# Kernel tuning notes

Measured on AMD Instinct MI355X. Metric: run time of the kernel, lower is better.

Reference implementation:

```python
import jax, jax.numpy as jnp
import numpy as np

REG_MAX = 16
NC = 80
TOPK = 10
ALPHA = 1.0
BETA = 6.0
BOX_W, CLS_W, DFL_W = 7.5, 0.5, 1.5
IMG = 1280.0


def _ciou(b1, b2, eps=1e-7):
    # b1, b2: [..., 4] xyxy, broadcastable
    b1x1, b1y1, b1x2, b1y2 = b1[..., 0], b1[..., 1], b1[..., 2], b1[..., 3]
    b2x1, b2y1, b2x2, b2y2 = b2[..., 0], b2[..., 1], b2[..., 2], b2[..., 3]
    w1, h1 = b1x2 - b1x1, b1y2 - b1y1
    w2, h2 = b2x2 - b2x1, b2y2 - b2y1
    inter = (jnp.maximum(jnp.minimum(b1x2, b2x2) - jnp.maximum(b1x1, b2x1), 0.0) *
             jnp.maximum(jnp.minimum(b1y2, b2y2) - jnp.maximum(b1y1, b2y1), 0.0))
    union = w1 * h1 + w2 * h2 - inter + eps
    iou = inter / union
    cw = jnp.maximum(b1x2, b2x2) - jnp.minimum(b1x1, b2x1)
    ch = jnp.maximum(b1y2, b2y2) - jnp.minimum(b1y1, b2y1)
    c2 = cw * cw + ch * ch + eps
    rho2 = ((b2x1 + b2x2 - b1x1 - b1x2) ** 2 + (b2y1 + b2y2 - b1y1 - b1y2) ** 2) / 4.0
    v = (4.0 / np.pi ** 2) * (jnp.arctan(w2 / (h2 + eps)) - jnp.arctan(w1 / (h1 + eps))) ** 2
    alpha = jax.lax.stop_gradient(v / (v - iou + (1.0 + eps)))
    return iou - (rho2 / c2 + v * alpha)


def _loss(p0, p1, p2, gt_boxes, gt_labels, strides):
    preds = [p0, p1, p2]
    B = p0.shape[0]
    aps, sts, pds, pcs = [], [], [], []
    for i, p in enumerate(preds):
        H, W = p.shape[2], p.shape[3]
        gy, gx = jnp.meshgrid(jnp.arange(H, dtype=p.dtype) + 0.5,
                              jnp.arange(W, dtype=p.dtype) + 0.5, indexing='ij')
        aps.append(jnp.stack([gx.ravel(), gy.ravel()], -1))          # [HW,2] feat units
        sts.append(jnp.ones((H * W, 1), p.dtype) * strides[i])       # [HW,1]
        pds.append(p[:, :4 * REG_MAX].reshape(B, 4, REG_MAX, H * W).transpose(0, 3, 1, 2))
        pcs.append(p[:, 4 * REG_MAX:].transpose(0, 2, 3, 1).reshape(B, H * W, NC))
    ap = jnp.concatenate(aps)                 # [N,2]
    st = jnp.concatenate(sts)                 # [N,1]
    pred_dist = jnp.concatenate(pds, axis=1)  # [B,N,4,R]
    pred_cls = jnp.concatenate(pcs, axis=1)   # [B,N,NC]
    proj = jnp.arange(REG_MAX, dtype=p0.dtype)
    M = gt_boxes.shape[1]
    N = ap.shape[0]

    def one_image(pd, pc, gb, gl):
        # decode boxes (image units)
        dist = jnp.einsum('nkr,r->nk', jax.nn.softmax(pd, -1), proj)        # [N,4]
        pred_boxes = jnp.concatenate([(ap - dist[:, :2]) * st,
                                      (ap + dist[:, 2:]) * st], -1)          # [N,4]
        # ---- TaskAlignedAssigner (no grad) ----
        sg = jax.lax.stop_gradient
        pb, ps, gbs = sg(pred_boxes), sg(jax.nn.sigmoid(pc)), sg(gb)
        ap_img = ap * st                                                     # [N,2]
        in_gt = ((ap_img[:, None, 0] >= gbs[None, :, 0]) & (ap_img[:, None, 0] <= gbs[None, :, 2]) &
                 (ap_img[:, None, 1] >= gbs[None, :, 1]) & (ap_img[:, None, 1] <= gbs[None, :, 3]))
        ious = jnp.maximum(_ciou(pb[:, None, :], gbs[None, :, :]), 0.0)      # [N,M]
        align = (ps[:, gl] ** ALPHA) * (ious ** BETA) * in_gt
        align = align / (align.max(0, keepdims=True) + 1e-9)
        align = align * (ious > 0.1)
        # topk anchors per GT; anchor takes the GT with max masked score
        #  sequential loop with strict '>' updates)
        vals, idx = jax.lax.top_k(align.T, TOPK)                             # [M,TOPK]
        masked = jnp.zeros((M, N), align.dtype).at[
            jnp.arange(M)[:, None], idx].set(jnp.where(vals > 0, vals, 0.0))
        col = masked.T                                                       # [N,M]
        best_gt = jnp.argmax(col, 1)
        best_score = col.max(1)
        fg = (best_score > 0).astype(pd.dtype)                               # [N]
        num_fg = jnp.maximum(fg.sum(), 1.0)
        labels = gl[best_gt]
        boxes = gbs[best_gt]
        # ---- box (CIoU) loss over fg ----
        box_loss = ((1.0 - _ciou(pred_boxes, boxes)) * fg).sum() / num_fg
        # ---- DFL loss over fg ----
        t = jnp.concatenate([ap - boxes[:, :2] / st, boxes[:, 2:] / st - ap], -1)
        t = jnp.clip(t, 0.0, REG_MAX - 1 - 0.01)   # box2dist clamp
        t = jnp.clip(t, 0.0, REG_MAX - 1e-4)       # DFLLoss clamp
        left = jnp.floor(t).astype(jnp.int32)
        right = jnp.minimum(left + 1, REG_MAX - 1)
        wl = right.astype(t.dtype) - t
        wr = t - left.astype(t.dtype)
        logp = jax.nn.log_softmax(pd, -1)                                    # [N,4,R]
        ce_l = -jnp.take_along_axis(logp, left[..., None], -1)[..., 0]
        ce_r = -jnp.take_along_axis(logp, right[..., None], -1)[..., 0]
        dfl_loss = ((ce_l * wl + ce_r * wr) * fg[:, None]).sum() / (num_fg * 4.0)
        # ---- cls BCE-with-logits over all anchors ----
        cls_t = jax.nn.one_hot(labels, NC, dtype=pc.dtype) * (best_score * fg)[:, None]
        cls_loss = (jnp.logaddexp(0.0, pc) - pc * cls_t).sum(1).mean()
        has_fg = (fg.sum() > 0).astype(pd.dtype)
        return box_loss * has_fg, cls_loss * has_fg, dfl_loss * has_fg

    bl, cl, dl = jax.vmap(one_image)(pred_dist, pred_cls, gt_boxes, gt_labels)
    return BOX_W * bl.sum() + CLS_W * cl.sum() + DFL_W * dl.sum()


def setup_inputs() -> dict:
    key = jax.random.key(0)
    ks = jax.random.split(key, 6)
    p0 = jax.random.normal(ks[0], (8, 144, 160, 160), jnp.float32)
    p1 = jax.random.normal(ks[1], (8, 144, 80, 80), jnp.float32)
    p2 = jax.random.normal(ks[2], (8, 144, 40, 40), jnp.float32)
    cxcy = jax.random.uniform(ks[3], (8, 32, 2), minval=64.0, maxval=IMG - 64.0)
    wh = jax.random.uniform(ks[4], (8, 32, 2), minval=16.0, maxval=256.0)
    gt_boxes = jnp.clip(jnp.concatenate([cxcy - wh / 2, cxcy + wh / 2], -1), 0.0, IMG)
    gt_labels = jax.random.randint(ks[5], (8, 32), 0, NC)
    strides = jnp.array([8.0, 16.0, 32.0], jnp.float32)
    return {"p0": p0, "p1": p1, "p2": p2, "gt_boxes": gt_boxes,
            "gt_labels": gt_labels, "strides": strides}


def reference(p0, p1, p2, gt_boxes, gt_labels, strides):
    return _loss(p0, p1, p2, gt_boxes, gt_labels, strides)
```

## Files before the change

### kernel.cpp

```cpp
#include <hip/hip_runtime.h>
#include <cstdint>

#define NANCHOR 33600
#define BATCH   8
#define MGT     32
#define NCLS    80
#define MAXFG   (BATCH * MGT * 10)

struct AInfo {
    const float* ch0;
    int   hw;
    float apx, apy, st;
};

__device__ __forceinline__ AInfo anchor_info(const float* p0, const float* p1,
                                             const float* p2, int b, int n) {
    AInfo r;
    if (n < 25600) {
        int nn = n;
        r.ch0 = p0 + (size_t)b * (144 * 25600) + nn;
        r.hw = 25600; r.st = 8.f;
        r.apx = (float)(nn % 160) + 0.5f;
        r.apy = (float)(nn / 160) + 0.5f;
    } else if (n < 32000) {
        int nn = n - 25600;
        r.ch0 = p1 + (size_t)b * (144 * 6400) + nn;
        r.hw = 6400; r.st = 16.f;
        r.apx = (float)(nn % 80) + 0.5f;
        r.apy = (float)(nn / 80) + 0.5f;
    } else {
        int nn = n - 32000;
        r.ch0 = p2 + (size_t)b * (144 * 1600) + nn;
        r.hw = 1600; r.st = 32.f;
        r.apx = (float)(nn % 40) + 0.5f;
        r.apy = (float)(nn / 40) + 0.5f;
    }
    return r;
}

__device__ __forceinline__ float ciou_f(float b1x1, float b1y1, float b1x2, float b1y2,
                                        float g1x, float g1y, float g2x, float g2y) {
    const float eps = 1e-7f;
    float w1 = b1x2 - b1x1, h1 = b1y2 - b1y1;
    float w2 = g2x - g1x,   h2 = g2y - g1y;
    float iw = fminf(b1x2, g2x) - fmaxf(b1x1, g1x);
    float ih = fminf(b1y2, g2y) - fmaxf(b1y1, g1y);
    float inter = fmaxf(iw, 0.f) * fmaxf(ih, 0.f);
    float uni = w1 * h1 + w2 * h2 - inter + eps;
    float iou = inter / uni;
    float cw = fmaxf(b1x2, g2x) - fminf(b1x1, g1x);
    float ch = fmaxf(b1y2, g2y) - fminf(b1y1, g1y);
    float c2 = cw * cw + ch * ch + eps;
    float dx = g1x + g2x - b1x1 - b1x2;
    float dy = g1y + g2y - b1y1 - b1y2;
    float rho2 = (dx * dx + dy * dy) * 0.25f;
    float t = atanf(w2 / (h2 + eps)) - atanf(w1 / (h1 + eps));
    float v = 0.40528473456935108577f * t * t;
    float alpha = v / (v - iou + (1.f + eps));
    return iou - (rho2 / c2 + v * alpha);
}

__device__ __forceinline__ float4 max4(float4 a, float4 b) {
    return make_float4(fmaxf(a.x, b.x), fmaxf(a.y, b.y), fmaxf(a.z, b.z), fmaxf(a.w, b.w));
}
__device__ __forceinline__ float fast_splus(float x) {
    return fmaxf(x, 0.f) + __logf(1.f + __expf(-fabsf(x)));
}


__global__ void k_init(float* acc) {
    acc[threadIdx.x] = 0.f;
}

__global__ __launch_bounds__(128) void k_decode(const float* __restrict__ p0,
                                                const float* __restrict__ p1,
                                                const float* __restrict__ p2,
                                                float2* __restrict__ pb2,
                                                unsigned long long* __restrict__ best,
                                                float* __restrict__ acc) {
    int b = blockIdx.y;
    int role = blockIdx.z;
    int t = blockIdx.x * 128 + threadIdx.x;

    if (role >= 2) {
        float sp = 0.f;
        if (t < NANCHOR / 4) {
            int n = t * 4;
            const float* ch0; int hw;
            if (n < 25600)      { ch0 = p0 + (size_t)b * (144 * 25600) + n;          hw = 25600; }
            else if (n < 32000) { ch0 = p1 + (size_t)b * (144 * 6400) + (n - 25600); hw = 6400; }
            else                { ch0 = p2 + (size_t)b * (144 * 1600) + (n - 32000); hw = 1600; }
            int c0 = 64 + (role - 2) * 40;
#pragma unroll 8
            for (int c = 0; c < 40; c++) {
                float4 x = *(const float4*)(ch0 + (size_t)(c0 + c) * hw);
                sp += fast_splus(x.x) + fast_splus(x.y) + fast_splus(x.z) + fast_splus(x.w);
            }
        }
#pragma unroll
        for (int o = 32; o > 0; o >>= 1) sp += __shfl_down(sp, o, 64);
        if ((threadIdx.x & 63) == 0) atomicAdd(&acc[b * 8 + 0], sp);
        return;
    }

    if (t >= NANCHOR / 4) return;
    int n = t * 4;
    const float* ch0; int hw; float st, apx, apy;
    if (n < 25600) {
        ch0 = p0 + (size_t)b * (144 * 25600) + n;
        hw = 25600; st = 8.f;
        apx = (float)(n % 160) + 0.5f; apy = (float)(n / 160) + 0.5f;
    } else if (n < 32000) {
        int nn = n - 25600;
        ch0 = p1 + (size_t)b * (144 * 6400) + nn;
        hw = 6400; st = 16.f;
        apx = (float)(nn % 80) + 0.5f; apy = (float)(nn / 80) + 0.5f;
    } else {
        int nn = n - 32000;
        ch0 = p2 + (size_t)b * (144 * 1600) + nn;
        hw = 1600; st = 32.f;
        apx = (float)(nn % 40) + 0.5f; apy = (float)(nn / 40) + 0.5f;
    }

    int k0 = role * 2;
    float d[2][4];
#pragma unroll
    for (int kk = 0; kk < 2; kk++) {
        float4 v[16];
#pragma unroll
        for (int r = 0; r < 16; r++)
            v[r] = *(const float4*)(ch0 + (size_t)((k0 + kk) * 16 + r) * hw);
        float4 mx = v[0];
#pragma unroll
        for (int r = 1; r < 16; r++) mx = max4(mx, v[r]);
        float4 s  = make_float4(0.f, 0.f, 0.f, 0.f);
        float4 sw = make_float4(0.f, 0.f, 0.f, 0.f);
#pragma unroll
        for (int r = 0; r < 16; r++) {
            float fr = (float)r;
            float ex = __expf(v[r].x - mx.x);
            float ey = __expf(v[r].y - mx.y);
            float ez = __expf(v[r].z - mx.z);
            float ew = __expf(v[r].w - mx.w);
            s.x += ex; s.y += ey; s.z += ez; s.w += ew;
            sw.x += ex * fr; sw.y += ey * fr; sw.z += ez * fr; sw.w += ew * fr;
        }
        d[kk][0] = sw.x / s.x; d[kk][1] = sw.y / s.y;
        d[kk][2] = sw.z / s.z; d[kk][3] = sw.w / s.w;
    }

    size_t base = (size_t)b * NANCHOR + n;
    if (role == 0) {
#pragma unroll
        for (int i = 0; i < 4; i++) {
            float ax = apx + (float)i;
            pb2[(base + i) * 2 + 0] = make_float2((ax - d[0][i]) * st, (apy - d[1][i]) * st);
        }
#pragma unroll
        for (int i = 0; i < 4; i++) best[base + i] = 0ull;
    } else {
#pragma unroll
        for (int i = 0; i < 4; i++) {
            float ax = apx + (float)i;
            pb2[(base + i) * 2 + 1] = make_float2((ax + d[0][i]) * st, (apy + d[1][i]) * st);
        }
    }
}

__global__ __launch_bounds__(256) void k_assign(const float* __restrict__ p0,
                                                const float* __restrict__ p1,
                                                const float* __restrict__ p2,
                                                const float4* __restrict__ pb,
                                                const float* __restrict__ gtb,
                                                const int* __restrict__ gtl,
                                                unsigned long long* __restrict__ best,
                                                float* __restrict__ acc,
                                                uint2* __restrict__ fglist) {
    int bm = blockIdx.x;
    int b = bm >> 5, m = bm & 31;
    const float* g = gtb + (size_t)(b * MGT + m) * 4;
    float g0 = g[0], g1 = g[1], g2 = g[2], g3 = g[3];
    int label = gtl[b * MGT + m];
    int tid = threadIdx.x;

    float tv[10];
    int   ti[10];
#pragma unroll
    for (int j = 0; j < 10; j++) { tv[j] = -1.f; ti[j] = 0x7fffffff; }
    float maxu = 0.f;

    const int   LW[3]   = {160, 80, 40};
    const int   LOFF[3] = {0, 25600, 32000};
    const float LST[3]  = {8.f, 16.f, 32.f};

    for (int l = 0; l < 3; l++) {
        float st = LST[l];
        int W = LW[l];
        float inv_st = 1.f / st;
        int ix0 = max(0,     (int)floorf(g0 * inv_st - 0.5f) - 1);
        int ix1 = min(W - 1, (int)ceilf (g2 * inv_st - 0.5f) + 1);
        int iy0 = max(0,     (int)floorf(g1 * inv_st - 0.5f) - 1);
        int iy1 = min(W - 1, (int)ceilf (g3 * inv_st - 0.5f) + 1);
        int nx = ix1 - ix0 + 1, ny = iy1 - iy0 + 1;
        if (nx <= 0 || ny <= 0) continue;
        int cnt = nx * ny;
        const float* lp = (l == 0) ? p0 : (l == 1) ? p1 : p2;
        int hw = W * W;
        const float* ch0 = lp + (size_t)b * 144 * hw;
        const float* pcls = ch0 + (size_t)(64 + label) * hw;

        for (int idx = tid; idx < cnt; idx += 256) {
            int iy = iy0 + idx / nx;
            int ix = ix0 + idx % nx;
            float ax = ((float)ix + 0.5f) * st;
            float ay = ((float)iy + 0.5f) * st;
            if (ax < g0 || ax > g2 || ay < g1 || ay > g3) continue;
            int nn = iy * W + ix;
            int n = LOFF[l] + nn;
            float4 box = pb[(size_t)b * NANCHOR + n];
            float c = ciou_f(box.x, box.y, box.z, box.w, g0, g1, g2, g3);
            float iou = fmaxf(c, 0.f);
            if (iou <= 0.f) continue;
            float pcv = pcls[nn];
            float ps = 1.f / (1.f + __expf(-pcv));
            float i2 = iou * iou;
            float a = ps * i2 * i2 * i2;
            maxu = fmaxf(maxu, a);
            if (iou > 0.1f && a > tv[9]) {
                tv[9] = a; ti[9] = n;
#pragma unroll
                for (int j = 9; j > 0; --j) {
                    if (tv[j] > tv[j - 1]) {
                        float tf = tv[j]; tv[j] = tv[j - 1]; tv[j - 1] = tf;
                        int   tt = ti[j]; ti[j] = ti[j - 1]; ti[j - 1] = tt;
                    }
                }
            }
        }
    }

    __shared__ float sval[2560];
    __shared__ int   sidx[2560];
    __shared__ float rv[256];
    __shared__ int   ra[256];
    __shared__ int   rs[256];
    __shared__ float smax[256];
    __shared__ int   winners[10];
    __shared__ int   nwin;

#pragma unroll
    for (int j = 0; j < 10; j++) {
        sval[tid * 10 + j] = tv[j];
        sidx[tid * 10 + j] = ti[j];
    }
    smax[tid] = maxu;
    if (tid == 0) nwin = 0;
    __syncthreads();
    for (int s = 128; s > 0; s >>= 1) {
        if (tid < s) smax[tid] = fmaxf(smax[tid], smax[tid + s]);
        __syncthreads();
    }
    float denom = smax[0] + 1e-9f;

    for (int r = 0; r < 10; r++) {
        float bv = -1.f; int ba = 0x7fffffff; int bs = -1;
#pragma unroll
        for (int j = 0; j < 10; j++) {
            int s0 = tid * 10 + j;
            float v = sval[s0]; int a0 = sidx[s0];
            if (v > bv || (v == bv && a0 < ba)) { bv = v; ba = a0; bs = s0; }
        }
        rv[tid] = bv; ra[tid] = ba; rs[tid] = bs;
        __syncthreads();
        for (int s = 128; s > 0; s >>= 1) {
            if (tid < s) {
                if (rv[tid + s] > rv[tid] ||
                    (rv[tid + s] == rv[tid] && ra[tid + s] < ra[tid])) {
                    rv[tid] = rv[tid + s]; ra[tid] = ra[tid + s]; rs[tid] = rs[tid + s];
                }
            }
            __syncthreads();
        }
        if (tid == 0 && rv[0] > 0.f) {
            float nv = rv[0] / denom;
            unsigned long long pk =
                ((unsigned long long)__float_as_uint(nv) << 32) |
                (unsigned long long)(31 - m);
            atomicMax(&best[(size_t)b * NANCHOR + ra[0]], pk);
            winners[nwin++] = ra[0];
            sval[rs[0]] = -1.f;
        }
        __syncthreads();
    }

    if (tid == 0 && nwin > 0) {
        unsigned int* list_cnt = (unsigned int*)(acc + 120);
        unsigned int base = atomicAdd(list_cnt, (unsigned int)nwin);
        for (int j = 0; j < nwin; j++)
            fglist[base + j] = make_uint2((unsigned int)(b * NANCHOR + winners[j]),
                                          (unsigned int)m);
    }
}

__global__ __launch_bounds__(256) void k_final(const float* __restrict__ p0,
                                               const float* __restrict__ p1,
                                               const float* __restrict__ p2,
                                               const float4* __restrict__ pb,
                                               const float* __restrict__ gtb,
                                               const int* __restrict__ gtl,
                                               const unsigned long long* __restrict__ best,
                                               const uint2* __restrict__ fglist,
                                               float* __restrict__ acc) {
    __shared__ float sacc[BATCH][4];
    int tid = threadIdx.x;
    if (tid < BATCH * 4) sacc[tid >> 2][tid & 3] = 0.f;
    __syncthreads();

    unsigned int cnt = *(const unsigned int*)(acc + 120);
    unsigned int i = blockIdx.x * 256 + tid;
    if (i < cnt) {
        uint2 e = fglist[i];
        int bn = (int)e.x, m = (int)e.y;
        unsigned long long pk = best[bn];
        if ((unsigned int)(pk & 0xffffffffull) == (unsigned int)(31 - m)) {
            int b = bn / NANCHOR, n = bn % NANCHOR;
            float score = __uint_as_float((unsigned int)(pk >> 32));
            const float* g = gtb + (size_t)(b * MGT + m) * 4;
            float g0 = g[0], g1 = g[1], g2 = g[2], g3 = g[3];
            int label = gtl[b * MGT + m];
            float4 box = pb[bn];
            float c = ciou_f(box.x, box.y, box.z, box.w, g0, g1, g2, g3);

            AInfo ai = anchor_info(p0, p1, p2, b, n);
            float inv_st = 1.f / ai.st;
            float t4[4] = { ai.apx - g0 * inv_st, ai.apy - g1 * inv_st,
                            g2 * inv_st - ai.apx, g3 * inv_st - ai.apy };
            float dfl = 0.f;
#pragma unroll
            for (int k = 0; k < 4; k++) {
                float t = fminf(fmaxf(t4[k], 0.f), 14.99f);
                int left = (int)floorf(t);
                int right = (left + 1 < 15) ? left + 1 : 15;
                float wl = (float)right - t;
                float wr = t - (float)left;
                float v[16];
                float mx = -1e30f;
#pragma unroll
                for (int r = 0; r < 16; r++) {
                    v[r] = ai.ch0[(size_t)(k * 16 + r) * ai.hw];
                    mx = fmaxf(mx, v[r]);
                }
                float s = 0.f;
#pragma unroll
                for (int r = 0; r < 16; r++) s += __expf(v[r] - mx);
                float lse = mx + __logf(s);
                dfl += (lse - v[left]) * wl + (lse - v[right]) * wr;
            }
            float pcv = ai.ch0[(size_t)(64 + label) * ai.hw];

            atomicAdd(&sacc[b][0], 1.f - c);
            atomicAdd(&sacc[b][1], dfl);
            atomicAdd(&sacc[b][2], pcv * score);
            atomicAdd(&sacc[b][3], 1.f);
        }
    }
    __syncthreads();
    if (tid < BATCH * 4) {
        float v = sacc[tid >> 2][tid & 3];
        if (v != 0.f) atomicAdd(&acc[(tid >> 2) * 8 + 1 + (tid & 3)], v);
    }
}

__global__ void k_combine(const float* __restrict__ acc, float* __restrict__ out) {
    if (blockIdx.x == 0 && threadIdx.x == 0) {
        float total = 0.f;
        for (int b = 0; b < BATCH; b++) {
            float nfr = acc[b * 8 + 4];
            float has = nfr > 0.f ? 1.f : 0.f;
            float nf = fmaxf(nfr, 1.f);
            float box_l = acc[b * 8 + 1] / nf;
            float cls_l = (acc[b * 8 + 0] - acc[b * 8 + 3]) / (float)NANCHOR;
            float dfl_l = acc[b * 8 + 2] / (nf * 4.f);
            total += has * (7.5f * box_l + 0.5f * cls_l + 1.5f * dfl_l);
        }
        out[0] = total;
    }
}

extern "C" void kernel_launch(void* const* d_in, const int* in_sizes, int n_in,
                              void* d_out, int out_size, void* d_ws, size_t ws_size,
                              hipStream_t stream) {
    (void)in_sizes; (void)n_in; (void)out_size; (void)ws_size;
    const float* p0  = (const float*)d_in[0];
    const float* p1  = (const float*)d_in[1];
    const float* p2  = (const float*)d_in[2];
    const float* gtb = (const float*)d_in[3];
    const int*   gtl = (const int*)d_in[4];

    char* ws = (char*)d_ws;
    unsigned long long* best = (unsigned long long*)ws;
    float4* pb = (float4*)(ws + (size_t)BATCH * NANCHOR * 8);
    float*  acc = (float*)(ws + (size_t)BATCH * NANCHOR * 8
                              + (size_t)BATCH * NANCHOR * 16);
    uint2* fglist = (uint2*)((char*)acc + 512);

    k_init   <<<1, 128, 0, stream>>>(acc);
    k_decode <<<dim3(66, BATCH, 4), 128, 0, stream>>>(p0, p1, p2, (float2*)pb, best, acc);
    k_assign <<<BATCH * MGT, 256, 0, stream>>>(p0, p1, p2, pb, gtb, gtl, best, acc, fglist);
    k_final  <<<(MAXFG + 255) / 256, 256, 0, stream>>>(p0, p1, p2, pb, gtb, gtl, best,
                                                       fglist, acc);
    k_combine<<<1, 64, 0, stream>>>(acc, (float*)d_out);
}
```

Measured before the change: 263.0 us.

## Split box decode per side into SoA planes and flatten softplus sweep

```diff
diff --git a/kernel.cpp b/kernel.cpp
--- a/kernel.cpp
+++ b/kernel.cpp
@@ -72,37 +72,39 @@
     acc[threadIdx.x] = 0.f;
 }
 
-__global__ __launch_bounds__(128) void k_decode(const float* __restrict__ p0,
+__global__ __launch_bounds__(256) void k_decode(const float* __restrict__ p0,
                                                 const float* __restrict__ p1,
                                                 const float* __restrict__ p2,
-                                                float2* __restrict__ pb2,
+                                                float4* __restrict__ px1,
+                                                float4* __restrict__ py1,
+                                                float4* __restrict__ px2,
+                                                float4* __restrict__ py2,
                                                 unsigned long long* __restrict__ best,
                                                 float* __restrict__ acc) {
     int b = blockIdx.y;
     int role = blockIdx.z;
-    int t = blockIdx.x * 128 + threadIdx.x;
-
-    if (role >= 2) {
+    int tid = threadIdx.x;
+
+    if (role >= 4) {
+        int sp_role = role - 4;
+        const float4* pc0 = (const float4*)(p0 + (size_t)b * 3686400 + 1638400);
+        const float4* pc1 = (const float4*)(p1 + (size_t)b * 921600  + 409600);
+        const float4* pc2 = (const float4*)(p2 + (size_t)b * 230400  + 102400);
         float sp = 0.f;
-        if (t < NANCHOR / 4) {
-            int n = t * 4;
-            const float* ch0; int hw;
-            if (n < 25600)      { ch0 = p0 + (size_t)b * (144 * 25600) + n;          hw = 25600; }
-            else if (n < 32000) { ch0 = p1 + (size_t)b * (144 * 6400) + (n - 25600); hw = 6400; }
-            else                { ch0 = p2 + (size_t)b * (144 * 1600) + (n - 32000); hw = 1600; }
-            int c0 = 64 + (role - 2) * 40;
-#pragma unroll 8
-            for (int c = 0; c < 40; c++) {
-                float4 x = *(const float4*)(ch0 + (size_t)(c0 + c) * hw);
-                sp += fast_splus(x.x) + fast_splus(x.y) + fast_splus(x.z) + fast_splus(x.w);
-            }
+        for (int g = (sp_role * 33 + blockIdx.x) * 256 + tid; g < 672000; g += 67584) {
+            float4 x;
+            if (g < 512000)      x = pc0[g];
+            else if (g < 640000) x = pc1[g - 512000];
+            else                 x = pc2[g - 640000];
+            sp += fast_splus(x.x) + fast_splus(x.y) + fast_splus(x.z) + fast_splus(x.w);
         }
 #pragma unroll
         for (int o = 32; o > 0; o >>= 1) sp += __shfl_down(sp, o, 64);
-        if ((threadIdx.x & 63) == 0) atomicAdd(&acc[b * 8 + 0], sp);
+        if ((tid & 63) == 0) atomicAdd(&acc[64 + b * 8 + sp_role], sp);
         return;
     }
 
+    int t = blockIdx.x * 256 + tid;
     if (t >= NANCHOR / 4) return;
     int n = t * 4;
     const float* ch0; int hw; float st, apx, apy;
@@ -122,55 +124,56 @@
         apx = (float)(nn % 40) + 0.5f; apy = (float)(nn / 40) + 0.5f;
     }
 
-    int k0 = role * 2;
-    float d[2][4];
-#pragma unroll
-    for (int kk = 0; kk < 2; kk++) {
-        float4 v[16];
-#pragma unroll
-        for (int r = 0; r < 16; r++)
-            v[r] = *(const float4*)(ch0 + (size_t)((k0 + kk) * 16 + r) * hw);
-        float4 mx = v[0];
-#pragma unroll
-        for (int r = 1; r < 16; r++) mx = max4(mx, v[r]);
-        float4 s  = make_float4(0.f, 0.f, 0.f, 0.f);
-        float4 sw = make_float4(0.f, 0.f, 0.f, 0.f);
-#pragma unroll
-        for (int r = 0; r < 16; r++) {
-            float fr = (float)r;
-            float ex = __expf(v[r].x - mx.x);
-            float ey = __expf(v[r].y - mx.y);
-            float ez = __expf(v[r].z - mx.z);
-            float ew = __expf(v[r].w - mx.w);
-            s.x += ex; s.y += ey; s.z += ez; s.w += ew;
-            sw.x += ex * fr; sw.y += ey * fr; sw.z += ez * fr; sw.w += ew * fr;
-        }
-        d[kk][0] = sw.x / s.x; d[kk][1] = sw.y / s.y;
-        d[kk][2] = sw.z / s.z; d[kk][3] = sw.w / s.w;
-    }
-
-    size_t base = (size_t)b * NANCHOR + n;
+    const float* side = ch0 + (size_t)(role * 16) * hw;
+    float4 v[16];
+#pragma unroll
+    for (int r = 0; r < 16; r++)
+        v[r] = *(const float4*)(side + (size_t)r * hw);
+    float4 mx = v[0];
+#pragma unroll
+    for (int r = 1; r < 16; r++) mx = max4(mx, v[r]);
+    float4 s  = make_float4(0.f, 0.f, 0.f, 0.f);
+    float4 sw = make_float4(0.f, 0.f, 0.f, 0.f);
+#pragma unroll
+    for (int r = 0; r < 16; r++) {
+        float fr = (float)r;
+        float ex = __expf(v[r].x - mx.x);
+        float ey = __expf(v[r].y - mx.y);
+        float ez = __expf(v[r].z - mx.z);
+        float ew = __expf(v[r].w - mx.w);
+        s.x += ex; s.y += ey; s.z += ez; s.w += ew;
+        sw.x += ex * fr; sw.y += ey * fr; sw.z += ez * fr; sw.w += ew * fr;
+    }
+    float d0 = sw.x / s.x, d1 = sw.y / s.y, d2 = sw.z / s.z, d3 = sw.w / s.w;
+
+    float4 res;
+    if (role == 0)      res = make_float4((apx + 0.f - d0) * st, (apx + 1.f - d1) * st,
+                                          (apx + 2.f - d2) * st, (apx + 3.f - d3) * st);
+    else if (role == 1) res = make_float4((apy - d0) * st, (apy - d1) * st,
+                                          (apy - d2) * st, (apy - d3) * st);
+    else if (role == 2) res = make_float4((apx + 0.f + d0) * st, (apx + 1.f + d1) * st,
+                                          (apx + 2.f + d2) * st, (apx + 3.f + d3) * st);
+    else                res = make_float4((apy + d0) * st, (apy + d1) * st,
+                                          (apy + d2) * st, (apy + d3) * st);
+
+    size_t gi = ((size_t)b * NANCHOR + n) >> 2;
+    float4* dst = (role == 0) ? px1 : (role == 1) ? py1 : (role == 2) ? px2 : py2;
+    dst[gi] = res;
+
     if (role == 0) {
-#pragma unroll
-        for (int i = 0; i < 4; i++) {
-            float ax = apx + (float)i;
-            pb2[(base + i) * 2 + 0] = make_float2((ax - d[0][i]) * st, (apy - d[1][i]) * st);
-        }
-#pragma unroll
-        for (int i = 0; i < 4; i++) best[base + i] = 0ull;
-    } else {
-#pragma unroll
-        for (int i = 0; i < 4; i++) {
-            float ax = apx + (float)i;
-            pb2[(base + i) * 2 + 1] = make_float2((ax + d[0][i]) * st, (apy + d[1][i]) * st);
-        }
+        ulonglong2* bq = (ulonglong2*)(best + (size_t)b * NANCHOR + n);
+        bq[0] = make_ulonglong2(0ull, 0ull);
+        bq[1] = make_ulonglong2(0ull, 0ull);
     }
 }
 
 __global__ __launch_bounds__(256) void k_assign(const float* __restrict__ p0,
                                                 const float* __restrict__ p1,
                                                 const float* __restrict__ p2,
-                                                const float4* __restrict__ pb,
+                                                const float* __restrict__ px1,
+                                                const float* __restrict__ py1,
+                                                const float* __restrict__ px2,
+                                                const float* __restrict__ py2,
                                                 const float* __restrict__ gtb,
                                                 const int* __restrict__ gtl,
                                                 unsigned long long* __restrict__ best,
@@ -217,8 +220,8 @@
             if (ax < g0 || ax > g2 || ay < g1 || ay > g3) continue;
             int nn = iy * W + ix;
             int n = LOFF[l] + nn;
-            float4 box = pb[(size_t)b * NANCHOR + n];
-            float c = ciou_f(box.x, box.y, box.z, box.w, g0, g1, g2, g3);
+            size_t bn = (size_t)b * NANCHOR + n;
+            float c = ciou_f(px1[bn], py1[bn], px2[bn], py2[bn], g0, g1, g2, g3);
             float iou = fmaxf(c, 0.f);
             if (iou <= 0.f) continue;
             float pcv = pcls[nn];
@@ -294,7 +297,7 @@
     }
 
     if (tid == 0 && nwin > 0) {
-        unsigned int* list_cnt = (unsigned int*)(acc + 120);
+        unsigned int* list_cnt = (unsigned int*)(acc + 63);
         unsigned int base = atomicAdd(list_cnt, (unsigned int)nwin);
         for (int j = 0; j < nwin; j++)
             fglist[base + j] = make_uint2((unsigned int)(b * NANCHOR + winners[j]),
@@ -305,7 +308,10 @@
 __global__ __launch_bounds__(256) void k_final(const float* __restrict__ p0,
                                                const float* __restrict__ p1,
                                                const float* __restrict__ p2,
-                                               const float4* __restrict__ pb,
+                                               const float* __restrict__ px1,
+                                               const float* __restrict__ py1,
+                                               const float* __restrict__ px2,
+                                               const float* __restrict__ py2,
                                                const float* __restrict__ gtb,
                                                const int* __restrict__ gtl,
                                                const unsigned long long* __restrict__ best,
@@ -316,7 +322,7 @@
     if (tid < BATCH * 4) sacc[tid >> 2][tid & 3] = 0.f;
     __syncthreads();
 
-    unsigned int cnt = *(const unsigned int*)(acc + 120);
+    unsigned int cnt = *(const unsigned int*)(acc + 63);
     unsigned int i = blockIdx.x * 256 + tid;
     if (i < cnt) {
         uint2 e = fglist[i];
@@ -328,8 +334,7 @@
             const float* g = gtb + (size_t)(b * MGT + m) * 4;
             float g0 = g[0], g1 = g[1], g2 = g[2], g3 = g[3];
             int label = gtl[b * MGT + m];
-            float4 box = pb[bn];
-            float c = ciou_f(box.x, box.y, box.z, box.w, g0, g1, g2, g3);
+            float c = ciou_f(px1[bn], py1[bn], px2[bn], py2[bn], g0, g1, g2, g3);
 
             AInfo ai = anchor_info(p0, p1, p2, b, n);
             float inv_st = 1.f / ai.st;
@@ -375,11 +380,13 @@
     if (blockIdx.x == 0 && threadIdx.x == 0) {
         float total = 0.f;
         for (int b = 0; b < BATCH; b++) {
+            float sp = 0.f;
+            for (int j = 0; j < 8; j++) sp += acc[64 + b * 8 + j];
             float nfr = acc[b * 8 + 4];
             float has = nfr > 0.f ? 1.f : 0.f;
             float nf = fmaxf(nfr, 1.f);
             float box_l = acc[b * 8 + 1] / nf;
-            float cls_l = (acc[b * 8 + 0] - acc[b * 8 + 3]) / (float)NANCHOR;
+            float cls_l = (sp - acc[b * 8 + 3]) / (float)NANCHOR;
             float dfl_l = acc[b * 8 + 2] / (nf * 4.f);
             total += has * (7.5f * box_l + 0.5f * cls_l + 1.5f * dfl_l);
         }
@@ -397,17 +404,22 @@
     const float* gtb = (const float*)d_in[3];
     const int*   gtl = (const int*)d_in[4];
 
+    const size_t BN = (size_t)BATCH * NANCHOR;
     char* ws = (char*)d_ws;
     unsigned long long* best = (unsigned long long*)ws;
-    float4* pb = (float4*)(ws + (size_t)BATCH * NANCHOR * 8);
-    float*  acc = (float*)(ws + (size_t)BATCH * NANCHOR * 8
-                              + (size_t)BATCH * NANCHOR * 16);
-    uint2* fglist = (uint2*)((char*)acc + 512);
-
-    k_init   <<<1, 128, 0, stream>>>(acc);
-    k_decode <<<dim3(66, BATCH, 4), 128, 0, stream>>>(p0, p1, p2, (float2*)pb, best, acc);
-    k_assign <<<BATCH * MGT, 256, 0, stream>>>(p0, p1, p2, pb, gtb, gtl, best, acc, fglist);
-    k_final  <<<(MAXFG + 255) / 256, 256, 0, stream>>>(p0, p1, p2, pb, gtb, gtl, best,
-                                                       fglist, acc);
+    float* px1 = (float*)(ws + BN * 8);
+    float* py1 = px1 + BN;
+    float* px2 = py1 + BN;
+    float* py2 = px2 + BN;
+    float* acc = py2 + BN;
+    uint2* fglist = (uint2*)(acc + 256);
+
+    k_init   <<<1, 256, 0, stream>>>(acc);
+    k_decode <<<dim3(33, BATCH, 12), 256, 0, stream>>>(p0, p1, p2,
+                (float4*)px1, (float4*)py1, (float4*)px2, (float4*)py2, best, acc);
+    k_assign <<<BATCH * MGT, 256, 0, stream>>>(p0, p1, p2, px1, py1, px2, py2,
+                                               gtb, gtl, best, acc, fglist);
+    k_final  <<<(MAXFG + 255) / 256, 256, 0, stream>>>(p0, p1, p2, px1, py1, px2, py2,
+                                                       gtb, gtl, best, fglist, acc);
     k_combine<<<1, 64, 0, stream>>>(acc, (float*)d_out);
 }
```

Result: slower. 296.7 us (+12.8%).
